# Performance work log

Measured on AMD Instinct MI355X. Metric: run time of the kernel, lower is better.

Reference implementation:

```python
import jax, jax.numpy as jnp
import numpy as np

DIM = 256
NUM_HEADS = 8
HEAD_DIM = DIM // NUM_HEADS
CPB_HIDDEN = 512
B, N = 2, 2304
TABLE = 9025  # (2*48-1)**2


def _l2norm(t, eps=1e-12):
    # matches torch F.normalize(dim=-1): x / max(||x||, eps)
    n = jnp.sqrt(jnp.sum(t * t, axis=-1, keepdims=True))
    return t / jnp.maximum(n, eps)


def setup_inputs() -> dict:
    key = jax.random.key(0)
    ks = jax.random.split(key, 12)
    x = jax.random.normal(ks[0], (B, N, DIM), dtype=jnp.float32)
    relative_pos_index = jax.random.randint(ks[1], (N, N), 0, TABLE, dtype=jnp.int64)
    relative_coords_table = jax.random.uniform(ks[2], (TABLE, 2), dtype=jnp.float32) * 2.0 - 1.0
    seq_length_scale = jnp.ones((1,), dtype=jnp.float32) * jnp.log2(jnp.float32(N))
    padding_mask = jnp.zeros((B, N), dtype=jnp.int32)
    s = 0.02
    W_qkv = jax.random.normal(ks[3], (3 * DIM, DIM), dtype=jnp.float32) * s
    b_qkv = jnp.zeros((3 * DIM,), dtype=jnp.float32)
    # temperature init: log(exp(1/0.24) - 1) so softplus(temperature) = 1/0.24
    temperature = jnp.full((NUM_HEADS, 1, 1), float(np.log(np.expm1(1.0 / 0.24))), dtype=jnp.float32)
    query_embedding = jax.random.normal(ks[4], (NUM_HEADS, 1, HEAD_DIM), dtype=jnp.float32) * s
    W_proj = jax.random.normal(ks[5], (DIM, DIM), dtype=jnp.float32) * s
    b_proj = jnp.zeros((DIM,), dtype=jnp.float32)
    W_cpb1 = jax.random.normal(ks[6], (CPB_HIDDEN, 2), dtype=jnp.float32) * s
    b_cpb1 = jnp.zeros((CPB_HIDDEN,), dtype=jnp.float32)
    W_cpb2 = jax.random.normal(ks[7], (NUM_HEADS, CPB_HIDDEN), dtype=jnp.float32) * s
    b_cpb2 = jnp.zeros((NUM_HEADS,), dtype=jnp.float32)
    return {
        'x': x, 'relative_pos_index': relative_pos_index,
        'relative_coords_table': relative_coords_table,
        'seq_length_scale': seq_length_scale, 'padding_mask': padding_mask,
        'W_qkv': W_qkv, 'b_qkv': b_qkv, 'temperature': temperature,
        'query_embedding': query_embedding, 'W_proj': W_proj, 'b_proj': b_proj,
        'W_cpb1': W_cpb1, 'b_cpb1': b_cpb1, 'W_cpb2': W_cpb2, 'b_cpb2': b_cpb2,
    }


def reference(x, relative_pos_index, relative_coords_table, seq_length_scale,
              padding_mask, W_qkv, b_qkv, temperature, query_embedding,
              W_proj, b_proj, W_cpb1, b_cpb1, W_cpb2, b_cpb2):
    Bx, Nx, C = x.shape
    h, d = NUM_HEADS, HEAD_DIM
    # qkv projection -> (B, 3h, N, d); first h heads = q, then k, then v
    qkv = (jnp.einsum('bnc,oc->bno', x, W_qkv) + b_qkv)
    qkv = qkv.reshape(Bx, Nx, 3 * h, d).transpose(0, 2, 1, 3)
    q, k, v = qkv[:, :h], qkv[:, h:2 * h], qkv[:, 2 * h:]
    # CPB relative bias: (T,2) -> (T,h) -> (h,N,N) via gather
    hid = jax.nn.relu(relative_coords_table @ W_cpb1.T + b_cpb1)
    tab = hid @ W_cpb2.T + b_cpb2                    # (T, h)
    rel_bias = tab.T[:, relative_pos_index.reshape(-1)].reshape(h, Nx, Nx)
    # cosine-sim attention with learned query embedding + softplus temperature
    scale = jax.nn.softplus(temperature) * seq_length_scale[0]   # (h,1,1)
    qn = (_l2norm(q) + query_embedding) * scale                  # (B,h,N,d)
    kn = _l2norm(k)
    attn = jnp.einsum('bhnd,bhmd->bhnm', qn, kn) + rel_bias
    attn = jax.nn.softmax(attn, axis=-1)
    out = jnp.einsum('bhnm,bhmd->bhnd', attn, v)
    out = out.transpose(0, 2, 1, 3).reshape(Bx, Nx, C)
    out = out @ W_proj.T + b_proj
    return out
```

## Files before the change

kernel.cpp:

```cpp
#include <hip/hip_runtime.h>
#include <math.h>

#define DIMC 256
#define NHEADS 8
#define HDIM 32
#define CPBH 512
#define BB 2
#define NSEQ 2304
#define TAB 9025
#define TABP 9040
#define RTOT (BB*NHEADS*NSEQ)
#define SPLITS 4
#define MSP (NSEQ/SPLITS)
#define PBS 36
#define NCHUNK (NSEQ/32)
#define LOG2E 1.44269504088896340736f

#define IDXP_ELEMS    (NSEQ * NCHUNK * 16)
#define IDXP4_BLOCKS  (IDXP_ELEMS / 1024)
#define CPB_BLOCKS    ((TAB + 63) / 64)
#define QKV_BLOCKS    (12 * 72)

typedef unsigned short ushort;
typedef __attribute__((ext_vector_type(8))) short short8;
typedef __attribute__((ext_vector_type(4))) short short4v;
typedef __attribute__((ext_vector_type(4))) float f32x4;
typedef __attribute__((ext_vector_type(4))) unsigned uint4v;

#define MFMA16(a,b,c) __builtin_amdgcn_mfma_f32_16x16x32_bf16((a),(b),(c),0,0,0)

#define GL16(SRC, DST) __builtin_amdgcn_global_load_lds( \
    (const __attribute__((address_space(1))) void*)(SRC), \
    (__attribute__((address_space(3))) void*)(DST), 16, 0, 0)

__device__ __forceinline__ ushort f2bf(float x) {
  unsigned u = __float_as_uint(x);
  u += 0x7FFFu + ((u >> 16) & 1u);
  return (ushort)(u >> 16);
}
__device__ __forceinline__ float bf2f(ushort b) {
  return __uint_as_float(((unsigned)b) << 16);
}
__device__ __forceinline__ float fexp2(float x) {
#if defined(__has_builtin)
#if __has_builtin(__builtin_amdgcn_exp2f)
  return __builtin_amdgcn_exp2f(x);
#else
  return exp2f(x);
#endif
#else
  return exp2f(x);
#endif
}
__device__ __forceinline__ unsigned pack_trunc(float p0, float p1) {
  return __builtin_amdgcn_perm(__float_as_uint(p1), __float_as_uint(p0), 0x07060302u);
}
__device__ __forceinline__ void cvt8(const float* __restrict__ p, short8* hi, short8* lo) {
  float4 v0 = *(const float4*)p;
  float4 v1 = *(const float4*)(p + 4);
  float vv[8] = {v0.x, v0.y, v0.z, v0.w, v1.x, v1.y, v1.z, v1.w};
  short8 h, l;
#pragma unroll
  for (int i = 0; i < 8; ++i) {
    ushort hh = f2bf(vv[i]);
    h[i] = (short)hh;
    l[i] = (short)f2bf(vv[i] - bf2f(hh));
  }
  *hi = h; *lo = l;
}

__launch_bounds__(256)
__global__ void pack_kernel(const int* __restrict__ idx, unsigned* __restrict__ idxP) {
  int t4 = blockIdx.x * 256 + threadIdx.x;
  int grp = t4 >> 4;
  int ch = grp % NCHUNK;
  int n4 = grp / NCHUNK;
  int m = ch * 32 + (t4 & 15);
  unsigned o[4];
#pragma unroll
  for (int i = 0; i < 4; ++i) {
    unsigned lo = (unsigned)idx[(size_t)(n4 * 4 + i) * NSEQ + m];
    unsigned hi = (unsigned)idx[(size_t)(n4 * 4 + i) * NSEQ + m + 16];
    o[i] = lo | (hi << 16);
  }
  *(uint4*)&idxP[(size_t)t4 * 4] = *(const uint4*)o;
}

__launch_bounds__(256)
__global__ void pre_kernel(const float* __restrict__ x, const float* __restrict__ wq,
                           const float* __restrict__ tbl, const float* __restrict__ W1,
                           const float* __restrict__ b1, const float* __restrict__ W2,
                           const float* __restrict__ b2,
                           const float* __restrict__ bias, const float* __restrict__ temp,
                           const float* __restrict__ sls, const float* __restrict__ qe,
                           ushort* __restrict__ qhi, ushort* __restrict__ qlo,
                           ushort* __restrict__ khi, ushort* __restrict__ klo,
                           ushort* __restrict__ vT, ushort* __restrict__ tabBf) {
  __shared__ __align__(16) ushort smemu[33792];
  int blk = blockIdx.x;
  int tid = threadIdx.x;

  if (blk < CPB_BLOCKS) {
    float* smem = (float*)smemu;
    float* w1b = smem;
    float* w2t = smem + 2048;
    float* part = smem + 6144;
    for (int i = tid; i < CPBH; i += 256) {
      w1b[i * 4 + 0] = W1[2 * i];
      w1b[i * 4 + 1] = W1[2 * i + 1];
      w1b[i * 4 + 2] = b1[i];
      w1b[i * 4 + 3] = 0.f;
    }
    for (int i = tid; i < CPBH * NHEADS; i += 256)
      w2t[(i & (CPBH - 1)) * NHEADS + (i >> 9)] = W2[i];
    int tl = tid & 63, jc = tid >> 6;
    int t = blk * 64 + tl;
    bool valid = t < TAB;
    float c0 = 0.f, c1 = 0.f;
    if (valid) { c0 = tbl[2 * t]; c1 = tbl[2 * t + 1]; }
    __syncthreads();
    float acc[NHEADS];
#pragma unroll
    for (int h = 0; h < NHEADS; ++h) acc[h] = 0.f;
    for (int j = jc * 128; j < jc * 128 + 128; ++j) {
      float4 wv = *(const float4*)&w1b[j * 4];
      float hid = fmaxf(fmaf(c0, wv.x, fmaf(c1, wv.y, wv.z)), 0.f);
      float4 wa = *(const float4*)&w2t[j * NHEADS];
      float4 wb = *(const float4*)&w2t[j * NHEADS + 4];
      acc[0] = fmaf(hid, wa.x, acc[0]);
      acc[1] = fmaf(hid, wa.y, acc[1]);
      acc[2] = fmaf(hid, wa.z, acc[2]);
      acc[3] = fmaf(hid, wa.w, acc[3]);
      acc[4] = fmaf(hid, wb.x, acc[4]);
      acc[5] = fmaf(hid, wb.y, acc[5]);
      acc[6] = fmaf(hid, wb.z, acc[6]);
      acc[7] = fmaf(hid, wb.w, acc[7]);
    }
#pragma unroll
    for (int h = 0; h < NHEADS; ++h) part[((size_t)jc * 64 + tl) * NHEADS + h] = acc[h];
    __syncthreads();
    if (jc == 0 && valid) {
#pragma unroll
      for (int h = 0; h < NHEADS; ++h) {
        float s = b2[h];
#pragma unroll
        for (int p = 0; p < 4; ++p) s += part[((size_t)p * 64 + tl) * NHEADS + h];
        tabBf[h * TABP + t] = f2bf(s * LOG2E);
      }
    }
  } else {
    ushort* bsh = smemu;
    ushort* bsl = smemu + 64 * 264;
    float (*vbuf)[65] = (float(*)[65])smemu;
    int t = blk - CPB_BLOCKS;
    int n0 = (t % 12) * 64, m0 = (t / 12) * 64;
    int lane = tid & 63, w = tid >> 6;
    int g = lane >> 4, c = lane & 15;
    int mw = m0 + w * 16;
    const int K = DIMC;

    {
      int rr = tid >> 2, cq = (tid & 3) * 64;
#pragma unroll
      for (int j = 0; j < 64; j += 8) {
        short8 hh, ll;
        cvt8(&wq[(size_t)(n0 + rr) * K + cq + j], &hh, &ll);
        *(short8*)&bsh[rr * 264 + cq + j] = hh;
        *(short8*)&bsl[rr * 264 + cq + j] = ll;
      }
    }
    __syncthreads();

    f32x4 acc[4] = {{0,0,0,0},{0,0,0,0},{0,0,0,0},{0,0,0,0}};
#pragma unroll 2
    for (int k0 = 0; k0 < K; k0 += 32) {
      short8 ah, al;
      cvt8(&x[(size_t)(mw + c) * K + k0 + g * 8], &ah, &al);
#pragma unroll
      for (int nt = 0; nt < 4; ++nt) {
        int br = (nt * 16 + c) * 264 + k0 + g * 8;
        short8 bh = *(const short8*)&bsh[br];
        short8 bl = *(const short8*)&bsl[br];
        acc[nt] = MFMA16(ah, bh, acc[nt]);
        acc[nt] = MFMA16(al, bh, acc[nt]);
        acc[nt] = MFMA16(ah, bl, acc[nt]);
      }
    }
#pragma unroll
    for (int nt = 0; nt < 4; ++nt) {
      float bv = bias[n0 + nt * 16 + c];
#pragma unroll
      for (int r = 0; r < 4; ++r) acc[nt][r] += bv;
    }
    __syncthreads();

    int b = (m0 >= NSEQ) ? 1 : 0;
    int nb = m0 - b * NSEQ;
    int sect = n0 >> 8;
    int hloc = (n0 & 255) >> 5;

    if (sect < 2) {
#pragma unroll
      for (int H = 0; H < 2; ++H) {
        int head = hloc + H;
        float scale = (sect == 0) ? log1pf(expf(temp[head])) * sls[0] * LOG2E : 0.f;
#pragma unroll
        for (int r = 0; r < 4; ++r) {
          float ss = acc[2*H][r]*acc[2*H][r] + acc[2*H+1][r]*acc[2*H+1][r];
          ss += __shfl_xor(ss, 1);
          ss += __shfl_xor(ss, 2);
          ss += __shfl_xor(ss, 4);
          ss += __shfl_xor(ss, 8);
          float inv = 1.f / fmaxf(sqrtf(ss), 1e-12f);
#pragma unroll
          for (int half = 0; half < 2; ++half) {
            int d = half * 16 + c;
            float val = acc[2*H + half][r] * inv;
            if (sect == 0) val = (val + qe[head * HDIM + d]) * scale;
            vbuf[w * 16 + g * 4 + r][H * 32 + d] = val;
          }
        }
      }
      __syncthreads();
      int plane = tid >> 7;
      int seg = tid & 127;
      int head = seg >> 6, row = seg & 63;
      const float* srcrow = &vbuf[row][head * 32];
      ushort out16[32];
#pragma unroll
      for (int i = 0; i < 32; ++i) {
        float v = srcrow[i];
        ushort hh = f2bf(v);
        out16[i] = plane ? f2bf(v - bf2f(hh)) : hh;
      }
      ushort* dstp = plane ? (sect == 0 ? qlo : klo) : (sect == 0 ? qhi : khi);
      size_t off = ((size_t)(b * NHEADS + hloc + head) * NSEQ + nb + row) * HDIM;
#pragma unroll
      for (int q4 = 0; q4 < 4; ++q4)
        *(int4*)&dstp[off + q4 * 8] = ((int4*)out16)[q4];
    } else {
#pragma unroll
      for (int nt = 0; nt < 4; ++nt)
#pragma unroll
        for (int r = 0; r < 4; ++r)
          vbuf[w * 16 + g * 4 + r][nt * 16 + c] = acc[nt][r];
      __syncthreads();
      int hbase = (n0 - 512) >> 5;
#pragma unroll
      for (int it = 0; it < 16; ++it) {
        int dloc = (tid >> 6) * 16 + it;
        int p = tid & 63;
        int pp = p & 31;
        int nsrc = (p & 32) + (pp & 1) * 16 + (pp >> 1);
        float v = vbuf[nsrc][dloc];
        int head = hbase + (dloc >> 5), d = dloc & 31;
        vT[((size_t)((b * NHEADS + head) * HDIM + d)) * NSEQ + nb + p] = f2bf(v);
      }
    }
  }
}

__launch_bounds__(256)
__global__ void attn_kernel(const ushort* __restrict__ qhi, const ushort* __restrict__ qlo,
                            const ushort* __restrict__ khi, const ushort* __restrict__ klo,
                            const ushort* __restrict__ vT, const ushort* __restrict__ tabBf,
                            const unsigned* __restrict__ idxP,
                            float* __restrict__ pO, float* __restrict__ pL) {
  __shared__ ushort tbf[10240];
  __shared__ __align__(16) ushort pbuf[8][16 * PBS];
  __shared__ __align__(16) ushort stg[2][6144];
  int tid = threadIdx.x;
  int lane = tid & 63;
  int w = tid >> 6;

  int bid = blockIdx.x;
  int qb = bid >> 5;
  int k8 = bid & 7;
  int j4 = (bid >> 3) & 3;
  int y  = k8 + 8 * j4;
  int s = y & 3, h = y >> 2;

  const ushort* tsrc = tabBf + h * TABP;
#pragma unroll
  for (int i = 0; i < 5; ++i) {
    int off = i * 2048 + tid * 8;
    *(int4*)&tbf[off] = *(const int4*)&tsrc[off];
  }

  int g = lane >> 4, c = lane & 15;
  int q0 = qb * 64 + w * 16;
  int qg0 = q0 >> 2;
  size_t rowA = (size_t)h * NSEQ;
  size_t rowB = (size_t)(NHEADS + h) * NSEQ;
  int m0 = s * MSP;

  int su   = tid & 127;
  int srow = su & 31;
  int sslt = su >> 5;
  const ushort* kb0 = (tid < 128) ? khi : klo;
  const ushort* sA = kb0 + (rowA + m0 + srow) * HDIM + sslt * 8;
  const ushort* sB = kb0 + (rowB + m0 + srow) * HDIM + sslt * 8;
  const ushort* sV = vT + ((size_t)(((tid < 128) ? h : NHEADS + h) * HDIM + srow)) * NSEQ
                     + m0 + sslt * 8;
  unsigned dwb = (unsigned)(tid & 192) * 8;

#define STAGE(DP) do {                         \
    GL16(sA, (DP) + dwb);                      \
    GL16(sB, (DP) + 2048 + dwb);               \
    GL16(sV, (DP) + 4096 + dwb);               \
    sA += 32 * HDIM; sB += 32 * HDIM; sV += 32; \
  } while (0)

  short8 qAh = *(const short8*)&qhi[(rowA + q0 + c) * HDIM + g * 8];
  short8 qAl = *(const short8*)&qlo[(rowA + q0 + c) * HDIM + g * 8];
  short8 qBh = *(const short8*)&qhi[(rowB + q0 + c) * HDIM + g * 8];
  short8 qBl = *(const short8*)&qlo[(rowB + q0 + c) * HDIM + g * 8];

  unsigned oIb = (unsigned)(((unsigned)(qg0 + g) * NCHUNK + (m0 >> 5)) * 64 + c * 4);
  unsigned oI  = oIb;
  uint4v ia = __builtin_nontemporal_load((const uint4v*)&idxP[oI]);

  STAGE(&stg[0][0]);
  __syncthreads();

  short one = (c == 0) ? (short)0x3F80 : (short)0;
  short8 onesB = {one, one, one, one, one, one, one, one};

  f32x4 oa0 = {0,0,0,0}, oa1 = {0,0,0,0}, ob0 = {0,0,0,0}, ob1 = {0,0,0,0};
  f32x4 la = {0,0,0,0}, lb = {0,0,0,0};
  ushort* pba = pbuf[w * 2];
  ushort* pbb = pbuf[w * 2 + 1];

  int kbo = g * 256 + c * 8;
  int cur = 0;

  for (int mt = m0; mt < m0 + MSP; mt += 32) {
    bool lastit = (mt + 32 >= m0 + MSP);
    unsigned oIn = lastit ? oIb : oI + 64;
    uint4v ian = __builtin_nontemporal_load((const uint4v*)&idxP[oIn]);
    oI = oIn;
    if (!lastit) STAGE(&stg[cur ^ 1][0]);

    const ushort* S = &stg[cur][0];
    short8 ak0h = *(const short8*)&S[kbo];
    short8 ak1h = *(const short8*)&S[kbo + 128];
    short8 ak0l = *(const short8*)&S[1024 + kbo];
    short8 ak1l = *(const short8*)&S[1024 + kbo + 128];
    short8 bk0h = *(const short8*)&S[2048 + kbo];
    short8 bk1h = *(const short8*)&S[2048 + kbo + 128];
    short8 bk0l = *(const short8*)&S[3072 + kbo];
    short8 bk1l = *(const short8*)&S[3072 + kbo + 128];

    f32x4 sa0 = {0,0,0,0}, sa1 = {0,0,0,0}, sb0 = {0,0,0,0}, sb1 = {0,0,0,0};
    sa0 = MFMA16(qAh, ak0h, sa0);
    sa1 = MFMA16(qAh, ak1h, sa1);
    sb0 = MFMA16(qBh, bk0h, sb0);
    sb1 = MFMA16(qBh, bk1h, sb1);
    sa0 = MFMA16(qAl, ak0h, sa0);
    sa1 = MFMA16(qAl, ak1h, sa1);
    sb0 = MFMA16(qBl, bk0h, sb0);
    sb1 = MFMA16(qBl, bk1h, sb1);
    sa0 = MFMA16(qAh, ak0l, sa0);
    sa1 = MFMA16(qAh, ak1l, sa1);
    sb0 = MFMA16(qBh, bk0l, sb0);
    sb1 = MFMA16(qBh, bk1l, sb1);

    unsigned ip[4] = {ia.x, ia.y, ia.z, ia.w};
    float b0[4], b1[4];
#pragma unroll
    for (int r = 0; r < 4; ++r) {
      b0[r] = bf2f(tbf[ip[r] & 0xFFFF]);
      b1[r] = bf2f(tbf[ip[r] >> 16]);
    }
#pragma unroll
    for (int r = 0; r < 4; ++r) {
      float pA0 = fexp2(sa0[r] + b0[r]);
      float pA1 = fexp2(sa1[r] + b1[r]);
      *(unsigned*)&pba[(g * 4 + r) * PBS + 2 * c] = pack_trunc(pA0, pA1);
      float pB0 = fexp2(sb0[r] + b0[r]);
      float pB1 = fexp2(sb1[r] + b1[r]);
      *(unsigned*)&pbb[(g * 4 + r) * PBS + 2 * c] = pack_trunc(pB0, pB1);
    }

    short4v paA = *(const short4v*)&pba[c * PBS + g * 8];
    short4v paB = *(const short4v*)&pba[c * PBS + g * 8 + 4];
    short8 pfa = __builtin_shufflevector(paA, paB, 0, 1, 2, 3, 4, 5, 6, 7);
    short4v pbA = *(const short4v*)&pbb[c * PBS + g * 8];
    short4v pbB = *(const short4v*)&pbb[c * PBS + g * 8 + 4];
    short8 pfb = __builtin_shufflevector(pbA, pbB, 0, 1, 2, 3, 4, 5, 6, 7);

    short8 vf0 = *(const short8*)&S[4096 + kbo];
    short8 vf1 = *(const short8*)&S[4096 + kbo + 128];
    short8 wf0 = *(const short8*)&S[5120 + kbo];
    short8 wf1 = *(const short8*)&S[5120 + kbo + 128];

    oa0 = MFMA16(pfa, vf0, oa0);
    oa1 = MFMA16(pfa, vf1, oa1);
    ob0 = MFMA16(pfb, wf0, ob0);
    ob1 = MFMA16(pfb, wf1, ob1);
    la  = MFMA16(pfa, onesB, la);
    lb  = MFMA16(pfb, onesB, lb);

    ia = ian;
    __syncthreads();
    cur ^= 1;
  }
#undef STAGE

  size_t prowA = (size_t)s * RTOT + rowA;
  size_t prowB = (size_t)s * RTOT + rowB;
#pragma unroll
  for (int r = 0; r < 4; ++r) {
    size_t pra = prowA + q0 + g * 4 + r;
    __builtin_nontemporal_store(oa0[r], &pO[pra * HDIM + c]);
    __builtin_nontemporal_store(oa1[r], &pO[pra * HDIM + 16 + c]);
    size_t prb = prowB + q0 + g * 4 + r;
    __builtin_nontemporal_store(ob0[r], &pO[prb * HDIM + c]);
    __builtin_nontemporal_store(ob1[r], &pO[prb * HDIM + 16 + c]);
    if (c == 0) {
      __builtin_nontemporal_store(la[r], &pL[pra]);
      __builtin_nontemporal_store(lb[r], &pL[prb]);
    }
  }
}

#define ALD 264
__launch_bounds__(256)
__global__ void gemm_proj_fused(const float* __restrict__ pO, const float* __restrict__ pL,
                                const float* __restrict__ Wp,
                                const float* __restrict__ bias, float* __restrict__ C) {
  __shared__ __align__(16) ushort Ahs[32 * ALD];
  __shared__ __align__(16) ushort Als[32 * ALD];
  int tid = threadIdx.x;
  int m0 = blockIdx.x * 32;
  int b = (m0 >= NSEQ) ? 1 : 0;
  int nb = m0 - b * NSEQ;

  {
    int rr = tid >> 3;
    int q  = tid & 3;
    int hp = (tid >> 2) & 1;
    int n = nb + rr;
#pragma unroll
    for (int hh = 0; hh < 4; ++hh) {
      int h = hp * 4 + hh;
      size_t bhn = (size_t)(b * NHEADS + h) * NSEQ + n;
      float L = 0.f;
#pragma unroll
      for (int sp = 0; sp < SPLITS; ++sp) L += pL[(size_t)sp * RTOT + bhn];
      float inv = 1.f / L;
      float a[8] = {0.f, 0.f, 0.f, 0.f, 0.f, 0.f, 0.f, 0.f};
#pragma unroll
      for (int sp = 0; sp < SPLITS; ++sp) {
        const float* src = &pO[((size_t)sp * RTOT + bhn) * HDIM + q * 8];
        float4 v0 = *(const float4*)&src[0];
        float4 v1 = *(const float4*)&src[4];
        a[0] += v0.x; a[1] += v0.y; a[2] += v0.z; a[3] += v0.w;
        a[4] += v1.x; a[5] += v1.y; a[6] += v1.z; a[7] += v1.w;
      }
      ushort hi8[8], lo8[8];
#pragma unroll
      for (int i = 0; i < 8; ++i) {
        float v = a[i] * inv;
        ushort hh2 = f2bf(v);
        hi8[i] = hh2;
        lo8[i] = f2bf(v - bf2f(hh2));
      }
      int k = h * 32 + q * 8;
      *(int4*)&Ahs[rr * ALD + k] = *(int4*)hi8;
      *(int4*)&Als[rr * ALD + k] = *(int4*)lo8;
    }
  }
  __syncthreads();

  int lane = tid & 63, w = tid >> 6;
  int g = lane >> 4, c = lane & 15;
  int n0 = w * 64;
  f32x4 acc[2][4] = {};
  for (int k0 = 0; k0 < DIMC; k0 += 32) {
    short8 bfh[4], bfl[4];
#pragma unroll
    for (int nt = 0; nt < 4; ++nt)
      cvt8(&Wp[(size_t)(n0 + nt * 16 + c) * DIMC + k0 + g * 8], &bfh[nt], &bfl[nt]);
#pragma unroll
    for (int mt = 0; mt < 2; ++mt) {
      short8 ah = *(const short8*)&Ahs[(mt * 16 + c) * ALD + k0 + g * 8];
      short8 al = *(const short8*)&Als[(mt * 16 + c) * ALD + k0 + g * 8];
#pragma unroll
      for (int nt = 0; nt < 4; ++nt) {
        acc[mt][nt] = MFMA16(ah, bfh[nt], acc[mt][nt]);
        acc[mt][nt] = MFMA16(al, bfh[nt], acc[mt][nt]);
        acc[mt][nt] = MFMA16(ah, bfl[nt], acc[mt][nt]);
      }
    }
  }
#pragma unroll
  for (int nt = 0; nt < 4; ++nt) {
    float bv = bias[n0 + nt * 16 + c];
#pragma unroll
    for (int mt = 0; mt < 2; ++mt)
#pragma unroll
      for (int r = 0; r < 4; ++r)
        C[(size_t)(m0 + mt * 16 + g * 4 + r) * DIMC + n0 + nt * 16 + c] = acc[mt][nt][r] + bv;
  }
}

extern "C" void kernel_launch(void* const* d_in, const int* in_sizes, int n_in,
                              void* d_out, int out_size, void* d_ws, size_t ws_size,
                              hipStream_t stream) {
  const float* x    = (const float*)d_in[0];
  const int*   idx  = (const int*)d_in[1];
  const float* tbl  = (const float*)d_in[2];
  const float* sls  = (const float*)d_in[3];
  const float* Wqkv = (const float*)d_in[5];
  const float* bqkv = (const float*)d_in[6];
  const float* temp = (const float*)d_in[7];
  const float* qe   = (const float*)d_in[8];
  const float* Wp   = (const float*)d_in[9];
  const float* bp   = (const float*)d_in[10];
  const float* W1   = (const float*)d_in[11];
  const float* b1   = (const float*)d_in[12];
  const float* W2   = (const float*)d_in[13];
  const float* b2   = (const float*)d_in[14];

  float* ws   = (float*)d_ws;
  float* pO   = ws;
  float* pL   = pO + (size_t)SPLITS * RTOT * HDIM;
  unsigned* idxP = (unsigned*)(pL + (size_t)SPLITS * RTOT);
  ushort* u   = (ushort*)(idxP + IDXP_ELEMS);
  ushort* qhi = u;                u += (size_t)RTOT * HDIM;
  ushort* qlo = u;                u += (size_t)RTOT * HDIM;
  ushort* khi = u;                u += (size_t)RTOT * HDIM;
  ushort* klo = u;                u += (size_t)RTOT * HDIM;
  ushort* vT  = u;                u += (size_t)RTOT * HDIM;
  ushort* tabBf = u;              u += 73728;
  float* out  = (float*)d_out;

  pack_kernel<<<dim3(IDXP4_BLOCKS), dim3(256), 0, stream>>>(idx, idxP);
  pre_kernel<<<dim3(CPB_BLOCKS + QKV_BLOCKS), dim3(256), 0, stream>>>(
      x, Wqkv, tbl, W1, b1, W2, b2, bqkv, temp, sls, qe,
      qhi, qlo, khi, klo, vT, tabBf);
  attn_kernel<<<dim3((NSEQ / 64) * NHEADS * SPLITS), dim3(256), 0, stream>>>(
      qhi, qlo, khi, klo, vT, tabBf, idxP, pO, pL);
  gemm_proj_fused<<<dim3((BB * NSEQ) / 32), dim3(256), 0, stream>>>(
      pO, pL, Wp, bp, out);
}
```

Measured before the change: 202.6 us.

## Process two 16-row query tiles per wave in attention kernel

Each wave now handles 32 query rows instead of 16, so every block covers 128 queries and the grid is halved. Each staged K/V tile and each bias-table load into LDS is reused across twice as many queries, which lowers LDS staging and global traffic per unit of work. The cost is higher register and LDS pressure, fewer blocks to fill the GPU (576 instead of 1152), and nontemporal loads and stores swapped for plain ones.

```diff
diff --git a/kernel.cpp b/kernel.cpp
--- a/kernel.cpp
+++ b/kernel.cpp
@@ -25,7 +25,6 @@
 typedef __attribute__((ext_vector_type(8))) short short8;
 typedef __attribute__((ext_vector_type(4))) short short4v;
 typedef __attribute__((ext_vector_type(4))) float f32x4;
-typedef __attribute__((ext_vector_type(4))) unsigned uint4v;
 
 #define MFMA16(a,b,c) __builtin_amdgcn_mfma_f32_16x16x32_bf16((a),(b),(c),0,0,0)
 
@@ -267,7 +266,7 @@
                             const unsigned* __restrict__ idxP,
                             float* __restrict__ pO, float* __restrict__ pL) {
   __shared__ ushort tbf[10240];
-  __shared__ __align__(16) ushort pbuf[8][16 * PBS];
+  __shared__ __align__(16) ushort pbuf[16][16 * PBS];
   __shared__ __align__(16) ushort stg[2][6144];
   int tid = threadIdx.x;
   int lane = tid & 63;
@@ -288,7 +287,7 @@
   }
 
   int g = lane >> 4, c = lane & 15;
-  int q0 = qb * 64 + w * 16;
+  int q0 = qb * 128 + w * 32;
   int qg0 = q0 >> 2;
   size_t rowA = (size_t)h * NSEQ;
   size_t rowB = (size_t)(NHEADS + h) * NSEQ;
@@ -311,14 +310,20 @@
     sA += 32 * HDIM; sB += 32 * HDIM; sV += 32; \
   } while (0)
 
-  short8 qAh = *(const short8*)&qhi[(rowA + q0 + c) * HDIM + g * 8];
-  short8 qAl = *(const short8*)&qlo[(rowA + q0 + c) * HDIM + g * 8];
-  short8 qBh = *(const short8*)&qhi[(rowB + q0 + c) * HDIM + g * 8];
-  short8 qBl = *(const short8*)&qlo[(rowB + q0 + c) * HDIM + g * 8];
-
+  short8 qA0h = *(const short8*)&qhi[(rowA + q0 + c) * HDIM + g * 8];
+  short8 qA0l = *(const short8*)&qlo[(rowA + q0 + c) * HDIM + g * 8];
+  short8 qA1h = *(const short8*)&qhi[(rowA + q0 + 16 + c) * HDIM + g * 8];
+  short8 qA1l = *(const short8*)&qlo[(rowA + q0 + 16 + c) * HDIM + g * 8];
+  short8 qB0h = *(const short8*)&qhi[(rowB + q0 + c) * HDIM + g * 8];
+  short8 qB0l = *(const short8*)&qlo[(rowB + q0 + c) * HDIM + g * 8];
+  short8 qB1h = *(const short8*)&qhi[(rowB + q0 + 16 + c) * HDIM + g * 8];
+  short8 qB1l = *(const short8*)&qlo[(rowB + q0 + 16 + c) * HDIM + g * 8];
+
+  const unsigned IOFF1 = 4u * NCHUNK * 64;
   unsigned oIb = (unsigned)(((unsigned)(qg0 + g) * NCHUNK + (m0 >> 5)) * 64 + c * 4);
   unsigned oI  = oIb;
-  uint4v ia = __builtin_nontemporal_load((const uint4v*)&idxP[oI]);
+  uint4 ia = *(const uint4*)&idxP[oI];
+  uint4 ja = *(const uint4*)&idxP[oI + IOFF1];
 
   STAGE(&stg[0][0]);
   __syncthreads();
@@ -326,10 +331,13 @@
   short one = (c == 0) ? (short)0x3F80 : (short)0;
   short8 onesB = {one, one, one, one, one, one, one, one};
 
-  f32x4 oa0 = {0,0,0,0}, oa1 = {0,0,0,0}, ob0 = {0,0,0,0}, ob1 = {0,0,0,0};
-  f32x4 la = {0,0,0,0}, lb = {0,0,0,0};
-  ushort* pba = pbuf[w * 2];
-  ushort* pbb = pbuf[w * 2 + 1];
+  f32x4 oa00 = {0,0,0,0}, oa01 = {0,0,0,0}, oa10 = {0,0,0,0}, oa11 = {0,0,0,0};
+  f32x4 ob00 = {0,0,0,0}, ob01 = {0,0,0,0}, ob10 = {0,0,0,0}, ob11 = {0,0,0,0};
+  f32x4 la0 = {0,0,0,0}, la1 = {0,0,0,0}, lb0 = {0,0,0,0}, lb1 = {0,0,0,0};
+  ushort* pba0 = pbuf[w * 4];
+  ushort* pba1 = pbuf[w * 4 + 1];
+  ushort* pbb0 = pbuf[w * 4 + 2];
+  ushort* pbb1 = pbuf[w * 4 + 3];
 
   int kbo = g * 256 + c * 8;
   int cur = 0;
@@ -337,7 +345,8 @@
   for (int mt = m0; mt < m0 + MSP; mt += 32) {
     bool lastit = (mt + 32 >= m0 + MSP);
     unsigned oIn = lastit ? oIb : oI + 64;
-    uint4v ian = __builtin_nontemporal_load((const uint4v*)&idxP[oIn]);
+    uint4 ian = *(const uint4*)&idxP[oIn];
+    uint4 jan = *(const uint4*)&idxP[oIn + IOFF1];
     oI = oIn;
     if (!lastit) STAGE(&stg[cur ^ 1][0]);
 
@@ -351,57 +360,82 @@
     short8 bk0l = *(const short8*)&S[3072 + kbo];
     short8 bk1l = *(const short8*)&S[3072 + kbo + 128];
 
-    f32x4 sa0 = {0,0,0,0}, sa1 = {0,0,0,0}, sb0 = {0,0,0,0}, sb1 = {0,0,0,0};
-    sa0 = MFMA16(qAh, ak0h, sa0);
-    sa1 = MFMA16(qAh, ak1h, sa1);
-    sb0 = MFMA16(qBh, bk0h, sb0);
-    sb1 = MFMA16(qBh, bk1h, sb1);
-    sa0 = MFMA16(qAl, ak0h, sa0);
-    sa1 = MFMA16(qAl, ak1h, sa1);
-    sb0 = MFMA16(qBl, bk0h, sb0);
-    sb1 = MFMA16(qBl, bk1h, sb1);
-    sa0 = MFMA16(qAh, ak0l, sa0);
-    sa1 = MFMA16(qAh, ak1l, sa1);
-    sb0 = MFMA16(qBh, bk0l, sb0);
-    sb1 = MFMA16(qBh, bk1l, sb1);
+    f32x4 sa0 = {0,0,0,0}, sa1 = {0,0,0,0}, ta0 = {0,0,0,0}, ta1 = {0,0,0,0};
+    f32x4 sb0 = {0,0,0,0}, sb1 = {0,0,0,0}, tb0 = {0,0,0,0}, tb1 = {0,0,0,0};
+    sa0 = MFMA16(qA0h, ak0h, sa0);
+    sa1 = MFMA16(qA0h, ak1h, sa1);
+    ta0 = MFMA16(qA1h, ak0h, ta0);
+    ta1 = MFMA16(qA1h, ak1h, ta1);
+    sb0 = MFMA16(qB0h, bk0h, sb0);
+    sb1 = MFMA16(qB0h, bk1h, sb1);
+    tb0 = MFMA16(qB1h, bk0h, tb0);
+    tb1 = MFMA16(qB1h, bk1h, tb1);
+    sa0 = MFMA16(qA0l, ak0h, sa0);
+    sa1 = MFMA16(qA0l, ak1h, sa1);
+    ta0 = MFMA16(qA1l, ak0h, ta0);
+    ta1 = MFMA16(qA1l, ak1h, ta1);
+    sb0 = MFMA16(qB0l, bk0h, sb0);
+    sb1 = MFMA16(qB0l, bk1h, sb1);
+    tb0 = MFMA16(qB1l, bk0h, tb0);
+    tb1 = MFMA16(qB1l, bk1h, tb1);
+    sa0 = MFMA16(qA0h, ak0l, sa0);
+    sa1 = MFMA16(qA0h, ak1l, sa1);
+    ta0 = MFMA16(qA1h, ak0l, ta0);
+    ta1 = MFMA16(qA1h, ak1l, ta1);
+    sb0 = MFMA16(qB0h, bk0l, sb0);
+    sb1 = MFMA16(qB0h, bk1l, sb1);
+    tb0 = MFMA16(qB1h, bk0l, tb0);
+    tb1 = MFMA16(qB1h, bk1l, tb1);
 
     unsigned ip[4] = {ia.x, ia.y, ia.z, ia.w};
-    float b0[4], b1[4];
+    unsigned jp[4] = {ja.x, ja.y, ja.z, ja.w};
 #pragma unroll
     for (int r = 0; r < 4; ++r) {
-      b0[r] = bf2f(tbf[ip[r] & 0xFFFF]);
-      b1[r] = bf2f(tbf[ip[r] >> 16]);
-    }
-#pragma unroll
-    for (int r = 0; r < 4; ++r) {
-      float pA0 = fexp2(sa0[r] + b0[r]);
-      float pA1 = fexp2(sa1[r] + b1[r]);
-      *(unsigned*)&pba[(g * 4 + r) * PBS + 2 * c] = pack_trunc(pA0, pA1);
-      float pB0 = fexp2(sb0[r] + b0[r]);
-      float pB1 = fexp2(sb1[r] + b1[r]);
-      *(unsigned*)&pbb[(g * 4 + r) * PBS + 2 * c] = pack_trunc(pB0, pB1);
-    }
-
-    short4v paA = *(const short4v*)&pba[c * PBS + g * 8];
-    short4v paB = *(const short4v*)&pba[c * PBS + g * 8 + 4];
-    short8 pfa = __builtin_shufflevector(paA, paB, 0, 1, 2, 3, 4, 5, 6, 7);
-    short4v pbA = *(const short4v*)&pbb[c * PBS + g * 8];
-    short4v pbB = *(const short4v*)&pbb[c * PBS + g * 8 + 4];
-    short8 pfb = __builtin_shufflevector(pbA, pbB, 0, 1, 2, 3, 4, 5, 6, 7);
+      float b0 = bf2f(tbf[ip[r] & 0xFFFF]);
+      float b1 = bf2f(tbf[ip[r] >> 16]);
+      *(unsigned*)&pba0[(g * 4 + r) * PBS + 2 * c] =
+          pack_trunc(fexp2(sa0[r] + b0), fexp2(sa1[r] + b1));
+      *(unsigned*)&pbb0[(g * 4 + r) * PBS + 2 * c] =
+          pack_trunc(fexp2(sb0[r] + b0), fexp2(sb1[r] + b1));
+      float d0 = bf2f(tbf[jp[r] & 0xFFFF]);
+      float d1 = bf2f(tbf[jp[r] >> 16]);
+      *(unsigned*)&pba1[(g * 4 + r) * PBS + 2 * c] =
+          pack_trunc(fexp2(ta0[r] + d0), fexp2(ta1[r] + d1));
+      *(unsigned*)&pbb1[(g * 4 + r) * PBS + 2 * c] =
+          pack_trunc(fexp2(tb0[r] + d0), fexp2(tb1[r] + d1));
+    }
+
+#define LOADP(PB, DST) do {                                             \
+    short4v pA_ = *(const short4v*)&(PB)[c * PBS + g * 8];              \
+    short4v pB_ = *(const short4v*)&(PB)[c * PBS + g * 8 + 4];          \
+    DST = __builtin_shufflevector(pA_, pB_, 0, 1, 2, 3, 4, 5, 6, 7);    \
+  } while (0)
+    short8 pfa0, pfa1, pfb0, pfb1;
+    LOADP(pba0, pfa0);
+    LOADP(pba1, pfa1);
+    LOADP(pbb0, pfb0);
+    LOADP(pbb1, pfb1);
+#undef LOADP
 
     short8 vf0 = *(const short8*)&S[4096 + kbo];
     short8 vf1 = *(const short8*)&S[4096 + kbo + 128];
     short8 wf0 = *(const short8*)&S[5120 + kbo];
     short8 wf1 = *(const short8*)&S[5120 + kbo + 128];
 
-    oa0 = MFMA16(pfa, vf0, oa0);
-    oa1 = MFMA16(pfa, vf1, oa1);
-    ob0 = MFMA16(pfb, wf0, ob0);
-    ob1 = MFMA16(pfb, wf1, ob1);
-    la  = MFMA16(pfa, onesB, la);
-    lb  = MFMA16(pfb, onesB, lb);
-
-    ia = ian;
+    oa00 = MFMA16(pfa0, vf0, oa00);
+    oa01 = MFMA16(pfa0, vf1, oa01);
+    oa10 = MFMA16(pfa1, vf0, oa10);
+    oa11 = MFMA16(pfa1, vf1, oa11);
+    ob00 = MFMA16(pfb0, wf0, ob00);
+    ob01 = MFMA16(pfb0, wf1, ob01);
+    ob10 = MFMA16(pfb1, wf0, ob10);
+    ob11 = MFMA16(pfb1, wf1, ob11);
+    la0  = MFMA16(pfa0, onesB, la0);
+    la1  = MFMA16(pfa1, onesB, la1);
+    lb0  = MFMA16(pfb0, onesB, lb0);
+    lb1  = MFMA16(pfb1, onesB, lb1);
+
+    ia = ian; ja = jan;
     __syncthreads();
     cur ^= 1;
   }
@@ -411,15 +445,21 @@
   size_t prowB = (size_t)s * RTOT + rowB;
 #pragma unroll
   for (int r = 0; r < 4; ++r) {
-    size_t pra = prowA + q0 + g * 4 + r;
-    __builtin_nontemporal_store(oa0[r], &pO[pra * HDIM + c]);
-    __builtin_nontemporal_store(oa1[r], &pO[pra * HDIM + 16 + c]);
-    size_t prb = prowB + q0 + g * 4 + r;
-    __builtin_nontemporal_store(ob0[r], &pO[prb * HDIM + c]);
-    __builtin_nontemporal_store(ob1[r], &pO[prb * HDIM + 16 + c]);
+    size_t pa0 = prowA + q0 + g * 4 + r;
+    pO[pa0 * HDIM + c]      = oa00[r];
+    pO[pa0 * HDIM + 16 + c] = oa01[r];
+    size_t pa1 = pa0 + 16;
+    pO[pa1 * HDIM + c]      = oa10[r];
+    pO[pa1 * HDIM + 16 + c] = oa11[r];
+    size_t pb0 = prowB + q0 + g * 4 + r;
+    pO[pb0 * HDIM + c]      = ob00[r];
+    pO[pb0 * HDIM + 16 + c] = ob01[r];
+    size_t pb1 = pb0 + 16;
+    pO[pb1 * HDIM + c]      = ob10[r];
+    pO[pb1 * HDIM + 16 + c] = ob11[r];
     if (c == 0) {
-      __builtin_nontemporal_store(la[r], &pL[pra]);
-      __builtin_nontemporal_store(lb[r], &pL[prb]);
+      pL[pa0] = la0[r]; pL[pa1] = la1[r];
+      pL[pb0] = lb0[r]; pL[pb1] = lb1[r];
     }
   }
 }
@@ -540,7 +580,7 @@
   pre_kernel<<<dim3(CPB_BLOCKS + QKV_BLOCKS), dim3(256), 0, stream>>>(
       x, Wqkv, tbl, W1, b1, W2, b2, bqkv, temp, sls, qe,
       qhi, qlo, khi, klo, vT, tabBf);
-  attn_kernel<<<dim3((NSEQ / 64) * NHEADS * SPLITS), dim3(256), 0, stream>>>(
+  attn_kernel<<<dim3((NSEQ / 128) * NHEADS * SPLITS), dim3(256), 0, stream>>>(
       qhi, qlo, khi, klo, vT, tabBf, idxP, pO, pL);
   gemm_proj_fused<<<dim3((BB * NSEQ) / 32), dim3(256), 0, stream>>>(
       pO, pL, Wp, bp, out);
```

Result: faster. 196.6 us (-3.0%).
